# Optimization experiments

Hardware: AMD Instinct MI355X
Metric: run time of the kernel (lower is better)

The kernel has to match this reference:

```python
import jax, jax.numpy as jnp
import numpy as np


def _pairwise_dist(x):
    # ||xi - xj||_2 via Gram trick: sq_ij = |xi|^2 + |xj|^2 - 2 xi.xj  (exact same math,
    # avoids the O(n^2*d) broadcast intermediate of the torch code)
    sq_norms = jnp.sum(x * x, axis=1)  # [n]
    gram = x @ x.T                      # [n, n]
    sq = jnp.maximum(sq_norms[:, None] + sq_norms[None, :] - 2.0 * gram, 0.0)
    # safe sqrt: zero distance (diagonal) stays exactly 0 with well-defined grad
    pos = sq > 0
    return jnp.where(pos, jnp.sqrt(jnp.where(pos, sq, 1.0)), 0.0)


def _double_center(a):
    # A = a - colmean - rowmean + grandmean
    return a - jnp.mean(a, axis=0)[None, :] - jnp.mean(a, axis=1)[:, None] + jnp.mean(a)


def setup_inputs() -> dict:
    key = jax.random.key(0)
    kx, ky = jax.random.split(key)
    x = jax.random.normal(kx, (8192, 128), dtype=jnp.float32)
    y = jax.random.normal(ky, (8192, 128), dtype=jnp.float32)
    return {"x": x, "y": y}


def reference(x, y):
    n = x.shape[0]
    A = _double_center(_pairwise_dist(x))  # [n, n]
    B = _double_center(_pairwise_dist(y))  # [n, n]
    inv_n2 = 1.0 / float(n * n)
    dcov2_xy = jnp.sum(A * B) * inv_n2
    dcov2_xx = jnp.sum(A * A) * inv_n2
    dcov2_yy = jnp.sum(B * B) * inv_n2
    dcor = -jnp.sqrt(dcov2_xy) / jnp.sqrt(jnp.sqrt(dcov2_xx) * jnp.sqrt(dcov2_yy))
    return dcor
```

## Files before the change

### kernel.cpp

```cpp
#include <hip/hip_runtime.h>


typedef float f32x4 __attribute__((ext_vector_type(4)));
typedef __bf16 bf16x8 __attribute__((ext_vector_type(8)));

#define NR 8192
#define D 128
#define TILE 128
#define GB 64
#define NT 2080

#define OFF_YB  2097152u
#define OFF_NX  4194304u
#define OFF_NY  (OFF_NX + 32768u)
#define OFF_RPX (OFF_NY + 32768u)
#define OFF_RPY (OFF_RPX + 2097152u)
#define OFF_PP  (OFF_RPY + 2097152u)
#define OFF_SB  (OFF_PP + 49920u)
#define WS_NEED (OFF_SB + 2560u)

#define GLOAD_LDS16(g, l)                                                  \
    __builtin_amdgcn_global_load_lds(                                      \
        (const __attribute__((address_space(1))) unsigned*)(g),            \
        (__attribute__((address_space(3))) unsigned*)(l), 16, 0, 0)

__device__ __forceinline__ unsigned short bf16_rne(float f) {
    union { float f; unsigned u; } c; c.f = f;
    unsigned u = c.u;
    u += 0x7FFFu + ((u >> 16) & 1u);
    return (unsigned short)(u >> 16);
}

__global__ __launch_bounds__(256) void prep_kernel(
    const float* __restrict__ x, const float* __restrict__ y,
    unsigned short* __restrict__ xb, unsigned short* __restrict__ yb,
    float* __restrict__ nx, float* __restrict__ ny)
{
    int gid = blockIdx.x * 256 + threadIdx.x;
    int wave = gid >> 6;
    int lane = threadIdx.x & 63;
    const float* src; unsigned short* db; float* dn; int row;
    if (wave < NR) { src = x; db = xb; dn = nx; row = wave; }
    else           { src = y; db = yb; dn = ny; row = wave - NR; }

    const float2 v = *reinterpret_cast<const float2*>(src + (size_t)row * D + lane * 2);
    float s = v.x * v.x + v.y * v.y;
    unsigned packed = (unsigned)bf16_rne(v.x) | ((unsigned)bf16_rne(v.y) << 16);
    *reinterpret_cast<unsigned*>(db + (size_t)row * D + lane * 2) = packed;
#pragma unroll
    for (int m = 1; m < 64; m <<= 1) s += __shfl_xor(s, m);
    if (lane == 0) dn[row] = s;
}

#define BSTEP(arr, S) {                                                    \
    const int b_ = (lrow >> (S)) & 1;                                      \
    _Pragma("unroll")                                                      \
    for (int i_ = 0; i_ < (8 >> (S)); ++i_) {                              \
        float k_ = b_ ? arr[2 * i_ + 1] : arr[2 * i_];                     \
        float s_ = b_ ? arr[2 * i_] : arr[2 * i_ + 1];                     \
        arr[i_] = k_ + __shfl_xor(s_, 1 << (S));                           \
    } }

__global__ __launch_bounds__(512) void dcor_main8(
    const unsigned short* __restrict__ xb, const unsigned short* __restrict__ yb,
    const float* __restrict__ nx, const float* __restrict__ ny,
    float* __restrict__ RPx, float* __restrict__ RPy,
    double* __restrict__ Pp )
{
    const int t = (blockIdx.x & 7) * (NT / 8) + (blockIdx.x >> 3);
    double qd = 2.0 * GB + 1.0;
    int bi = (int)((qd - sqrt(qd * qd - 8.0 * (double)t)) * 0.5);
    while (bi > 0 && bi * GB - bi * (bi - 1) / 2 > t) --bi;
    while ((bi + 1) * GB - (bi + 1) * bi / 2 <= t) ++bi;
    const int bj = bi + (t - (bi * GB - bi * (bi - 1) / 2));
    const bool diag = (bi == bj);

    __shared__ __align__(16) unsigned short Buf[2][TILE][64];
    __shared__ float nl[4][TILE];
    __shared__ float rsum[4][TILE];
    __shared__ float pr[3][8];

    const int tid  = threadIdx.x;
    const int lane = tid & 63, wid = tid >> 6;
    const int wr = wid >> 2, wc = wid & 3;
    const int lrow = lane & 15, lkb = lane >> 4;

    if (tid < TILE) {
        nl[0][tid] = nx[bi * TILE + tid];
        nl[1][tid] = nx[bj * TILE + tid];
        nl[2][tid] = ny[bi * TILE + tid];
        nl[3][tid] = ny[bj * TILE + tid];
        rsum[0][tid] = 0.f; rsum[1][tid] = 0.f;
        rsum[2][tid] = 0.f; rsum[3][tid] = 0.f;
    }

    auto stage = [&](int b, const unsigned short* srcb, int kc) {
        const char* gb = (const char*)srcb;
#pragma unroll
        for (int it = 0; it < 2; ++it) {
            int s = wid * 2 + it;
            int row = s * 8 + (lane >> 3);
            int c = (lane & 7) ^ (row & 7);
            int pr_ = (c < 4 ? bi : bj) * TILE + row;
            const char* g = gb + (size_t)pr_ * 256 + kc * 64 + (c & 3) * 16;
            GLOAD_LDS16(g, &Buf[b][s * 8][0]);
        }
    };

    int abyte[4], bbyte[2];
#pragma unroll
    for (int m = 0; m < 4; ++m) {
        int r = wr * 64 + m * 16 + lrow;
        abyte[m] = r * 128 + (lkb ^ (r & 7)) * 16;
    }
#pragma unroll
    for (int nf = 0; nf < 2; ++nf) {
        int r = wc * 32 + nf * 16 + lrow;
        bbyte[nf] = r * 128 + ((4 | lkb) ^ (r & 7)) * 16;
    }

    auto gram = [&](int b, f32x4 (&acc)[4][2]) {
        const char* base = (const char*)&Buf[b][0][0];
        bf16x8 a[4], bb[2];
#pragma unroll
        for (int m = 0; m < 4; ++m)
            a[m] = *reinterpret_cast<const bf16x8*>(base + abyte[m]);
#pragma unroll
        for (int nf = 0; nf < 2; ++nf)
            bb[nf] = *reinterpret_cast<const bf16x8*>(base + bbyte[nf]);
#pragma unroll
        for (int m = 0; m < 4; ++m)
#pragma unroll
            for (int nf = 0; nf < 2; ++nf)
                acc[m][nf] = __builtin_amdgcn_mfma_f32_16x16x32_bf16(
                    a[m], bb[nf], acc[m][nf], 0, 0, 0);
    };

    auto to_dist = [&](f32x4 (&acc)[4][2], const float* nRw, const float* nC) {
        const float nc0 = nC[wc * 32 + lrow];
        const float nc1 = nC[wc * 32 + 16 + lrow];
#pragma unroll
        for (int m = 0; m < 4; ++m) {
            float nr[4];
#pragma unroll
            for (int r = 0; r < 4; ++r)
                nr[r] = nRw[wr * 64 + m * 16 + lkb * 4 + r];
#pragma unroll
            for (int nf = 0; nf < 2; ++nf) {
                const float nc = nf ? nc1 : nc0;
#pragma unroll
                for (int r = 0; r < 4; ++r) {
                    float sq = nr[r] + nc - 2.f * acc[m][nf][r];
                    acc[m][nf][r] = __builtin_amdgcn_sqrtf(fmaxf(sq, 0.f));
                }
            }
        }
        if (diag) {
#pragma unroll
            for (int m = 0; m < 4; ++m)
#pragma unroll
                for (int nf = 0; nf < 2; ++nf)
#pragma unroll
                    for (int r = 0; r < 4; ++r) {
                        int row_l = wr * 64 + m * 16 + lkb * 4 + r;
                        int col_l = wc * 32 + nf * 16 + lrow;
                        if (row_l == col_l) acc[m][nf][r] = 0.f;
                    }
        }
    };

    const f32x4 fz = {0.f, 0.f, 0.f, 0.f};
    f32x4 accX[4][2], accY[4][2];
#pragma unroll
    for (int m = 0; m < 4; ++m)
#pragma unroll
        for (int nf = 0; nf < 2; ++nf) { accX[m][nf] = fz; accY[m][nf] = fz; }

    stage(0, xb, 0);
    __syncthreads();
    stage(1, xb, 1); gram(0, accX);
    __syncthreads();
    stage(0, xb, 2); gram(1, accX);
    __syncthreads();
    stage(1, xb, 3); gram(0, accX);
    __syncthreads();
    stage(0, yb, 0); gram(1, accX);
    to_dist(accX, nl[0], nl[1]);
    __syncthreads();
    stage(1, yb, 1); gram(0, accY);
    __syncthreads();
    stage(0, yb, 2); gram(1, accY);
    __syncthreads();
    stage(1, yb, 3); gram(0, accY);
    __syncthreads();
    gram(1, accY);
    to_dist(accY, nl[2], nl[3]);

    float pxy = 0.f, pxx = 0.f, pyy = 0.f;
    float ax[16], ay[16];
    float csx[2] = {0.f, 0.f}, csy[2] = {0.f, 0.f};
#pragma unroll
    for (int j = 0; j < 16; ++j) { ax[j] = 0.f; ay[j] = 0.f; }

#pragma unroll
    for (int m = 0; m < 4; ++m)
#pragma unroll
        for (int nf = 0; nf < 2; ++nf)
#pragma unroll
            for (int r = 0; r < 4; ++r) {
                float dx = accX[m][nf][r], dy = accY[m][nf][r];
                pxy += dx * dy;
                pxx += dx * dx;
                pyy += dy * dy;
                ax[m * 4 + r] += dx;  ay[m * 4 + r] += dy;
                csx[nf] += dx;        csy[nf] += dy;
            }

    BSTEP(ax, 0) BSTEP(ay, 0)
    BSTEP(ax, 1) BSTEP(ay, 1)
    BSTEP(ax, 2) BSTEP(ay, 2)
    BSTEP(ax, 3) BSTEP(ay, 3)
    {
        int row_l = wr * 64 + ((lrow >> 2) << 4) + (lkb << 2) + (lrow & 3);
        atomicAdd(&rsum[0][row_l], ax[0]);
        atomicAdd(&rsum[1][row_l], ay[0]);
    }
#pragma unroll
    for (int nf = 0; nf < 2; ++nf) {
        float vx = csx[nf], vy = csy[nf];
        vx += __shfl_xor(vx, 16); vx += __shfl_xor(vx, 32);
        vy += __shfl_xor(vy, 16); vy += __shfl_xor(vy, 32);
        if (lkb == 0) {
            int col_l = wc * 32 + nf * 16 + lrow;
            atomicAdd(&rsum[2][col_l], vx);
            atomicAdd(&rsum[3][col_l], vy);
        }
    }
#pragma unroll
    for (int m = 1; m < 64; m <<= 1) {
        pxy += __shfl_xor(pxy, m);
        pxx += __shfl_xor(pxx, m);
        pyy += __shfl_xor(pyy, m);
    }
    if (lane == 0) { pr[0][wid] = pxy; pr[1][wid] = pxx; pr[2][wid] = pyy; }
    __syncthreads();

    if (tid == 0) {
        double sxy = 0, sxx = 0, syy = 0;
#pragma unroll
        for (int w = 0; w < 8; ++w) {
            sxy += (double)pr[0][w]; sxx += (double)pr[1][w]; syy += (double)pr[2][w];
        }
        double sc = diag ? 1.0 : 2.0;
        Pp[t] = sxy * sc;
        Pp[NT + t] = sxx * sc;
        Pp[2 * NT + t] = syy * sc;
    }
    if (tid < TILE) {
        RPx[((size_t)bi * GB + bj) * TILE + tid] = rsum[0][tid];
        RPy[((size_t)bi * GB + bj) * TILE + tid] = rsum[1][tid];
        if (!diag) {
            RPx[((size_t)bj * GB + bi) * TILE + tid] = rsum[2][tid];
            RPy[((size_t)bj * GB + bi) * TILE + tid] = rsum[3][tid];
        }
    }
}

__global__ __launch_bounds__(128) void row_reduce2(
    const float* __restrict__ RPx, const float* __restrict__ RPy,
    double* __restrict__ SB )
{
    int b = blockIdx.x, t = threadIdx.x;
    double rx = 0.0, ry = 0.0;
    for (int k = 0; k < GB; ++k) {
        rx += (double)RPx[((size_t)b * GB + k) * TILE + t];
        ry += (double)RPy[((size_t)b * GB + k) * TILE + t];
    }
    double s0 = rx, s1 = ry, s2 = rx * ry, s3 = rx * rx, s4 = ry * ry;
#pragma unroll
    for (int m = 1; m < 64; m <<= 1) {
        s0 += __shfl_xor(s0, m); s1 += __shfl_xor(s1, m);
        s2 += __shfl_xor(s2, m); s3 += __shfl_xor(s3, m);
        s4 += __shfl_xor(s4, m);
    }
    __shared__ double sb[5][2];
    int lane = t & 63, w = t >> 6;
    if (lane == 0) { sb[0][w] = s0; sb[1][w] = s1; sb[2][w] = s2; sb[3][w] = s3; sb[4][w] = s4; }
    __syncthreads();
    if (t == 0)
#pragma unroll
        for (int i = 0; i < 5; ++i) SB[b * 5 + i] = sb[i][0] + sb[i][1];
}

__global__ __launch_bounds__(256) void dcor_final3(
    const double* __restrict__ SB, const double* __restrict__ Pp,
    unsigned* __restrict__ out)
{
    double sx = 0, sy = 0, sxy = 0, sxx = 0, syy = 0, pxy = 0, pxx = 0, pyy = 0;
    for (int b = threadIdx.x; b < GB; b += 256) {
        sx += SB[b * 5]; sy += SB[b * 5 + 1]; sxy += SB[b * 5 + 2];
        sxx += SB[b * 5 + 3]; syy += SB[b * 5 + 4];
    }
    for (int b = threadIdx.x; b < NT; b += 256) {
        pxy += Pp[b]; pxx += Pp[NT + b]; pyy += Pp[2 * NT + b];
    }
    __shared__ double red[8][4];
    int lane = threadIdx.x & 63, w = threadIdx.x >> 6;
#pragma unroll
    for (int m = 1; m < 64; m <<= 1) {
        sx += __shfl_xor(sx, m);  sy += __shfl_xor(sy, m);
        sxy += __shfl_xor(sxy, m); sxx += __shfl_xor(sxx, m); syy += __shfl_xor(syy, m);
        pxy += __shfl_xor(pxy, m); pxx += __shfl_xor(pxx, m); pyy += __shfl_xor(pyy, m);
    }
    if (lane == 0) {
        red[0][w] = sx;  red[1][w] = sy;  red[2][w] = sxy; red[3][w] = sxx;
        red[4][w] = syy; red[5][w] = pxy; red[6][w] = pxx; red[7][w] = pyy;
    }
    __syncthreads();
    if (threadIdx.x == 0) {
        sx  = red[0][0] + red[0][1] + red[0][2] + red[0][3];
        sy  = red[1][0] + red[1][1] + red[1][2] + red[1][3];
        sxy = red[2][0] + red[2][1] + red[2][2] + red[2][3];
        sxx = red[3][0] + red[3][1] + red[3][2] + red[3][3];
        syy = red[4][0] + red[4][1] + red[4][2] + red[4][3];
        pxy = red[5][0] + red[5][1] + red[5][2] + red[5][3];
        pxx = red[6][0] + red[6][1] + red[6][2] + red[6][3];
        pyy = red[7][0] + red[7][1] + red[7][2] + red[7][3];
        const double inv = 1.0 / (double)NR;
        double vxy = pxy - 2.0 * inv * sxy + sx * sy * inv * inv;
        double vxx = pxx - 2.0 * inv * sxx + sx * sx * inv * inv;
        double vyy = pyy - 2.0 * inv * syy + sy * sy * inv * inv;
        vxy = fmax(vxy, 0.0);
        vxx = fmax(vxx, 1e-30); vyy = fmax(vyy, 1e-30);
        double dcor = -sqrt(vxy) / sqrt(sqrt(vxx) * sqrt(vyy));
        unsigned short b = bf16_rne((float)dcor);
        out[0] = ((unsigned)b << 16) | (unsigned)b;
    }
}

extern "C" void kernel_launch(void* const* d_in, const int* in_sizes, int n_in,
                              void* d_out, int out_size, void* d_ws, size_t ws_size,
                              hipStream_t stream)
{
    const float* x = (const float*)d_in[0];
    const float* y = (const float*)d_in[1];
    char* ws = (char*)d_ws;
    unsigned short* xb = (unsigned short*)(ws);
    unsigned short* yb = (unsigned short*)(ws + OFF_YB);
    float* nx = (float*)(ws + OFF_NX);
    float* ny = (float*)(ws + OFF_NY);
    float* RPx = (float*)(ws + OFF_RPX);
    float* RPy = (float*)(ws + OFF_RPY);
    double* Pp = (double*)(ws + OFF_PP);
    double* SB = (double*)(ws + OFF_SB);

    prep_kernel<<<4096, 256, 0, stream>>>(x, y, xb, yb, nx, ny);
    dcor_main8<<<NT, 512, 0, stream>>>(xb, yb, nx, ny, RPx, RPy, Pp);
    row_reduce2<<<GB, 128, 0, stream>>>(RPx, RPy, SB);
    dcor_final3<<<1, 256, 0, stream>>>(SB, Pp, (unsigned*)d_out);
}
```

Before: 100.1 us.

## Deepen gram staging to four LDS buffers with vmcnt-based phase barriers

Grows the shared staging buffer from two to four K-chunk slots so three chunks are in flight before the first gram step. Full __syncthreads calls are replaced by explicit s_waitcnt vmcnt(N) plus a raw s_barrier, so each phase waits only for the chunk it needs. The aim is to hide global-to-LDS load latency behind MFMA work. In exchange it doubles LDS use, which may reduce blocks per CU, and correctness depends on the hand-set vmcnt counts matching the loads each stage issues.

Measured after the change: 93.30 us. 1.07x faster.

```diff
diff --git a/kernel.cpp b/kernel.cpp
--- a/kernel.cpp
+++ b/kernel.cpp
@@ -24,6 +24,13 @@
         (const __attribute__((address_space(1))) unsigned*)(g),            \
         (__attribute__((address_space(3))) unsigned*)(l), 16, 0, 0)
 
+#define PHASE_BAR(N)                                                       \
+    do {                                                                   \
+        asm volatile("s_waitcnt vmcnt(" #N ")" ::: "memory");              \
+        __builtin_amdgcn_sched_barrier(0);                                 \
+        __builtin_amdgcn_s_barrier();                                      \
+    } while (0)
+
 __device__ __forceinline__ unsigned short bf16_rne(float f) {
     union { float f; unsigned u; } c; c.f = f;
     unsigned u = c.u;
@@ -61,7 +68,7 @@
         arr[i_] = k_ + __shfl_xor(s_, 1 << (S));                           \
     } }
 
-__global__ __launch_bounds__(512) void dcor_main8(
+__global__ __launch_bounds__(512) void dcor_main9(
     const unsigned short* __restrict__ xb, const unsigned short* __restrict__ yb,
     const float* __restrict__ nx, const float* __restrict__ ny,
     float* __restrict__ RPx, float* __restrict__ RPy,
@@ -75,7 +82,7 @@
     const int bj = bi + (t - (bi * GB - bi * (bi - 1) / 2));
     const bool diag = (bi == bj);
 
-    __shared__ __align__(16) unsigned short Buf[2][TILE][64];
+    __shared__ __align__(16) unsigned short Buf[4][TILE][64];
     __shared__ float nl[4][TILE];
     __shared__ float rsum[4][TILE];
     __shared__ float pr[3][8];
@@ -176,24 +183,27 @@
 #pragma unroll
         for (int nf = 0; nf < 2; ++nf) { accX[m][nf] = fz; accY[m][nf] = fz; }
 
-    stage(0, xb, 0);
     __syncthreads();
-    stage(1, xb, 1); gram(0, accX);
-    __syncthreads();
-    stage(0, xb, 2); gram(1, accX);
-    __syncthreads();
-    stage(1, xb, 3); gram(0, accX);
-    __syncthreads();
-    stage(0, yb, 0); gram(1, accX);
+
+    stage(0, xb, 0); stage(1, xb, 1); stage(2, xb, 2);
+    PHASE_BAR(4);
+    gram(0, accX); stage(3, xb, 3);
+    PHASE_BAR(4);
+    gram(1, accX); stage(0, yb, 0);
+    PHASE_BAR(4);
+    gram(2, accX); stage(1, yb, 1);
+    PHASE_BAR(4);
+    gram(3, accX);
     to_dist(accX, nl[0], nl[1]);
-    __syncthreads();
-    stage(1, yb, 1); gram(0, accY);
-    __syncthreads();
-    stage(0, yb, 2); gram(1, accY);
-    __syncthreads();
-    stage(1, yb, 3); gram(0, accY);
-    __syncthreads();
+    stage(2, yb, 2);
+    PHASE_BAR(4);
+    gram(0, accY); stage(3, yb, 3);
+    PHASE_BAR(4);
     gram(1, accY);
+    PHASE_BAR(2);
+    gram(2, accY);
+    PHASE_BAR(0);
+    gram(3, accY);
     to_dist(accY, nl[2], nl[3]);
 
     float pxy = 0.f, pxx = 0.f, pyy = 0.f;
@@ -355,7 +365,7 @@
     double* SB = (double*)(ws + OFF_SB);
 
     prep_kernel<<<4096, 256, 0, stream>>>(x, y, xb, yb, nx, ny);
-    dcor_main8<<<NT, 512, 0, stream>>>(xb, yb, nx, ny, RPx, RPy, Pp);
+    dcor_main9<<<NT, 512, 0, stream>>>(xb, yb, nx, ny, RPx, RPy, Pp);
     row_reduce2<<<GB, 128, 0, stream>>>(RPx, RPy, SB);
     dcor_final3<<<1, 256, 0, stream>>>(SB, Pp, (unsigned*)d_out);
 }
```
